# Optimization experiments

Hardware: AMD Instinct MI355X
Metric: run time of the kernel (lower is better)

The kernel has to match this reference:

```python
import jax, jax.numpy as jnp
import numpy as np

FEATURE_MAPS = (38, 19, 10, 5, 3, 1)
BOXES_PER_LOC = (4, 6, 6, 6, 4, 4)
IMAGE_SIZE = 300
DEC_SIZE = 64  # WhatDecoder output resolution
MAX_OBJECTS = 10
Z_WHAT = 64


def _recon_indices():
    # Maps per-prior slots (8732) to per-location slots (1940), matching
    # Decoder.reconstruction_indices: each location index repeated boxes_per_loc times.
    idx, last = [], 0
    for fm, bpl in zip(FEATURE_MAPS, BOXES_PER_LOC):
        loc = np.arange(fm * fm) + last
        idx.append(np.repeat(loc, bpl))
        last = loc[-1] + 1
    return jnp.asarray(np.concatenate(idx), dtype=jnp.int32)


def _deconv2x2(x, W, b):
    # ConvTranspose2d(kernel=2, stride=2): each input pixel expands to a 2x2 block.
    n, c, h, w = x.shape
    o = W.shape[1]
    y = jnp.einsum('nchw,coab->nohawb', x, W).reshape(n, o, 2 * h, 2 * w)
    return y + b[None, :, None, None]


def _what_decoder(z, params):
    # z (M, Z_WHAT) -> (M, 3, 64, 64) in [0,1]
    x = z[:, :, None, None]
    nl = len(params)
    for i, (W, b) in enumerate(params):
        x = _deconv2x2(x, W, b)
        x = jax.nn.relu(x) if i < nl - 1 else jax.nn.sigmoid(x)
    return x


def _stn(images, z_where):
    # Spatial transformer: place (M,3,S,S) glyphs into IMAGE_SIZE canvas at box
    # z_where (M,4) = (cx,cy,w,h) in [0,1]; bilinear sampling, zeros padding.
    M, _, S, _ = images.shape
    cx, cy, w, h = (z_where[:, i] for i in range(4))
    # output pixel centers in normalized [-1,1] coords (align_corners=False)
    coords = (2.0 * jnp.arange(IMAGE_SIZE, dtype=images.dtype) + 1.0) / IMAGE_SIZE - 1.0
    xo = coords[None, None, :]
    yo = coords[None, :, None]
    eps = 1e-6
    u = (xo - (2.0 * cx - 1.0)[:, None, None]) / (w[:, None, None] + eps)  # (M,H,W)
    v = (yo - (2.0 * cy - 1.0)[:, None, None]) / (h[:, None, None] + eps)
    ix = ((u + 1.0) * S - 1.0) / 2.0  # input pixel coords
    iy = ((v + 1.0) * S - 1.0) / 2.0

    def sample_one(img, iy, ix):
        iy0 = jnp.floor(iy)
        ix0 = jnp.floor(ix)
        wy1 = iy - iy0
        wx1 = ix - ix0
        wy0 = 1.0 - wy1
        wx0 = 1.0 - wx1

        def g(y, x):
            yi = jnp.clip(y, 0, S - 1).astype(jnp.int32)
            xi = jnp.clip(x, 0, S - 1).astype(jnp.int32)
            valid = ((y >= 0) & (y < S) & (x >= 0) & (x < S)).astype(img.dtype)
            return img[:, yi, xi] * valid  # (3,H,W)

        return (g(iy0, ix0) * wy0 * wx0 + g(iy0, ix0 + 1) * wy0 * wx1
                + g(iy0 + 1, ix0) * wy1 * wx0 + g(iy0 + 1, ix0 + 1) * wy1 * wx1)

    return jax.vmap(sample_one)(images, iy, ix)  # (M,3,H,H)


def setup_inputs() -> dict:
    key = jax.random.key(0)
    ks = jax.random.split(key, 20)
    B, NLOC, NPRI = 16, 1940, 8732
    chans = (Z_WHAT, 256, 128, 64, 32, 16, 3)
    inp = {
        'z_what': jax.random.normal(ks[0], (B, NLOC, Z_WHAT), jnp.float32),
        'z_where': jax.random.uniform(ks[1], (B, NPRI, 4), jnp.float32),
        'z_present': jax.random.randint(ks[2], (B, NPRI, 1), 0, 2, jnp.int32),
        'z_depth': jax.random.normal(ks[3], (B, NLOC, 1), jnp.float32),
    }
    for i in range(6):
        ci, co = chans[i], chans[i + 1]
        inp[f'W{i}'] = jax.random.normal(ks[4 + i], (ci, co, 2, 2), jnp.float32) * 0.1
        inp[f'b{i}'] = jnp.zeros((co,), jnp.float32)
    return inp


def reference(z_what, z_where, z_present, z_depth,
              W0, b0, W1, b1, W2, b2, W3, b3, W4, b4, W5, b5):
    params = [(W0, b0), (W1, b1), (W2, b2), (W3, b3), (W4, b4), (W5, b5)]
    idx = _recon_indices()
    zw = z_what[:, idx]      # (B, P, D) ragged location->prior gather
    zd = z_depth[:, idx, 0]  # (B, P)
    order = jnp.argsort(-zd, axis=1)[:, :MAX_OBJECTS]  # depth sort, descending
    B, K = order.shape

    def gat(t):
        return jnp.take_along_axis(
            t, jnp.broadcast_to(order[:, :, None], (B, K, t.shape[-1])), axis=1)

    sw = gat(zw)            # (B,K,D)
    swr = gat(z_where)      # (B,K,4)
    sp = gat(z_present)     # (B,K,1)

    decoded = _what_decoder(sw.reshape(B * K, Z_WHAT), params)      # (B*K,3,64,64)
    transformed = _stn(decoded, swr.reshape(B * K, 4))              # (B*K,3,300,300)
    present = (sp == 1).astype(transformed.dtype).reshape(B * K, 1, 1, 1)
    objs = (transformed * present).reshape(B, K, 3, IMAGE_SIZE, IMAGE_SIZE)

    # z-buffer merge: per pixel, take first nonzero object in depth order
    nz = objs != 0.0
    first = nz & (jnp.cumsum(nz.astype(jnp.int32), axis=1) == 1)
    return jnp.sum(objs * first.astype(objs.dtype), axis=1)  # (B,3,300,300)
```

## Files before the change

kernel.cpp:

```cpp
#include <hip/hip_runtime.h>
#include <cmath>

#define NLOC 1940
#define NPRI 8732
#define BATCH 16
#define KOBJ 10

__device__ __forceinline__ void ins3(float v, int i,
    float& a0, float& a1, float& a2, int& j0, int& j1, int& j2)
{
    if (v > a0 || (v == a0 && i < j0)) { a2=a1; j2=j1; a1=a0; j1=j0; a0=v; j0=i; }
    else if (v > a1 || (v == a1 && i < j1)) { a2=a1; j2=j1; a1=v; j1=i; }
    else if (v > a2 || (v == a2 && i < j2)) { a2=v; j2=i; }
}

__device__ __forceinline__ float ix_chain(int x, float shift, float wh) {
    const float xo = __fsub_rn(__fdiv_rn(__fadd_rn(__fmul_rn(2.0f, (float)x), 1.0f), 300.0f), 1.0f);
    const float u  = __fdiv_rn(__fsub_rn(xo, shift), wh);
    return __fmul_rn(__fsub_rn(__fmul_rn(__fadd_rn(u, 1.0f), 64.0f), 1.0f), 0.5f);
}

__global__ __launch_bounds__(256) void prep_kernel(
    const float* __restrict__ W0, const float* __restrict__ W1, float* __restrict__ Wr,
    const float* __restrict__ z_what, const float* __restrict__ z_where,
    const int* __restrict__ z_present, const float* __restrict__ z_depth,
    float* __restrict__ gathered, float* __restrict__ paramsF, int* __restrict__ paramsI,
    int* __restrict__ obnd)
{
    __shared__ float sv[768];
    __shared__ int   si[768];
    __shared__ int   locs3[3];
    __shared__ int   sj_start[3], sj_bpl[3];
    __shared__ int   spres[10], sjj[10];
    __shared__ float szw[10][4];
    __shared__ float lpf[KOBJ][4];
    __shared__ int   lcnt;
    const int tid = threadIdx.x;

    if (blockIdx.x < 768) {
        const int idx = blockIdx.x * 256 + tid;
        if (idx < 65536) {
            int q = idx >> 14, rem = idx & 16383, c = rem >> 8, o = rem & 255;
            Wr[idx] = W0[(((c << 8) | o) << 2) + q];
        } else {
            int i2 = idx - 65536;
            int q = i2 >> 15, rem = i2 & 32767, c = rem >> 7, o = rem & 127;
            Wr[idx] = W1[(((c << 7) | o) << 2) + q];
        }
        return;
    }

    const int b = blockIdx.x - 768;
    float v0 = -INFINITY, v1 = -INFINITY, v2 = -INFINITY;
    int   i0 = NLOC, i1 = NLOC, i2 = NLOC;
    for (int i = tid; i < NLOC; i += 256) {
        float v = z_depth[b * NLOC + i];
        ins3(v, i, v0, v1, v2, i0, i1, i2);
    }
    sv[tid*3+0] = v0; sv[tid*3+1] = v1; sv[tid*3+2] = v2;
    si[tid*3+0] = i0; si[tid*3+1] = i1; si[tid*3+2] = i2;
    __syncthreads();
    for (int s = 128; s > 0; s >>= 1) {
        if (tid < s) {
            float a0 = sv[tid*3], a1 = sv[tid*3+1], a2 = sv[tid*3+2];
            int   j0 = si[tid*3], j1 = si[tid*3+1], j2 = si[tid*3+2];
            const int o = tid + s;
            ins3(sv[o*3+0], si[o*3+0], a0, a1, a2, j0, j1, j2);
            ins3(sv[o*3+1], si[o*3+1], a0, a1, a2, j0, j1, j2);
            ins3(sv[o*3+2], si[o*3+2], a0, a1, a2, j0, j1, j2);
            sv[tid*3] = a0; sv[tid*3+1] = a1; sv[tid*3+2] = a2;
            si[tid*3] = j0; si[tid*3+1] = j1; si[tid*3+2] = j2;
        }
        __syncthreads();
    }

    if (tid < 3) {
        int L = si[tid];
        locs3[tid] = L;
        int start, bpl;
        if (L < 1444)      { start = 4 * L;                 bpl = 4; }
        else if (L < 1805) { start = 5776 + 6 * (L - 1444); bpl = 6; }
        else if (L < 1905) { start = 7942 + 6 * (L - 1805); bpl = 6; }
        else if (L < 1930) { start = 8542 + 6 * (L - 1905); bpl = 6; }
        else if (L < 1939) { start = 8692 + 4 * (L - 1930); bpl = 4; }
        else               { start = 8728;                  bpl = 4; }
        sj_start[tid] = start; sj_bpl[tid] = bpl;
    }
    __syncthreads();
    if (tid < 10) {
        const int b0 = sj_bpl[0], b1 = sj_bpl[1];
        int j, o;
        if (tid < b0)           { j = 0; o = tid; }
        else if (tid < b0 + b1) { j = 1; o = tid - b0; }
        else                    { j = 2; o = tid - b0 - b1; }
        const int p = sj_start[j] + o;
        sjj[tid]   = j;
        spres[tid] = z_present[b * NPRI + p];
        const float4 zw = *reinterpret_cast<const float4*>(z_where + (b * NPRI + p) * 4);
        szw[tid][0] = zw.x; szw[tid][1] = zw.y; szw[tid][2] = zw.z; szw[tid][3] = zw.w;
    }
    __syncthreads();
    if (tid == 0) {
        int cnt = 0;
        for (int i = 0; i < 10; ++i) {
            if (spres[i] == 1) {
                float p0 = __fadd_rn(szw[i][2], 1e-6f);
                float p1 = __fadd_rn(szw[i][3], 1e-6f);
                float p2 = __fsub_rn(__fmul_rn(2.0f, szw[i][0]), 1.0f);
                float p3 = __fsub_rn(__fmul_rn(2.0f, szw[i][1]), 1.0f);
                float* pf = paramsF + (b * KOBJ + cnt) * 4;
                pf[0] = p0; pf[1] = p1; pf[2] = p2; pf[3] = p3;
                lpf[cnt][0] = p0; lpf[cnt][1] = p1; lpf[cnt][2] = p2; lpf[cnt][3] = p3;
                paramsI[b * 12 + 2 + cnt] = b * 3 + sjj[i];
                cnt++;
            }
        }
        paramsI[b * 12] = cnt;
        lcnt = cnt;
    }
    __syncthreads();
    if (tid < 4 * KOBJ) {
        const int k = tid >> 2, ty = tid & 3;
        if (k < lcnt) {
            const float wh = (ty < 2) ? lpf[k][0] : lpf[k][1];
            const float sh = (ty < 2) ? lpf[k][2] : lpf[k][3];
            int res;
            if ((ty & 1) == 0) {
                int lo = 0, hi = 300;
                while (lo < hi) { int m = (lo + hi) >> 1;
                    if (ix_chain(m, sh, wh) > -1.0f) hi = m; else lo = m + 1; }
                res = lo;
            } else {
                int lo = -1, hi = 299;
                while (lo < hi) { int m = (lo + hi + 1) >> 1;
                    if (ix_chain(m, sh, wh) < 64.0f) lo = m; else hi = m - 1; }
                res = lo;
            }
            obnd[(b * KOBJ + k) * 4 + ty] = res;
        }
    }
    if (tid < 192) {
        int j = tid >> 6, c = tid & 63;
        gathered[(b * 3 + j) * 64 + c] = z_what[(b * NLOC + locs3[j]) * 64 + c];
    }
}

__global__ __launch_bounds__(256) void dec_fused(
    const float* __restrict__ gathered, const float* __restrict__ Wr,
    const float* __restrict__ b0v, const float* __restrict__ b1v,
    const float* __restrict__ W2, const float* __restrict__ b2v,
    const float* __restrict__ W3, const float* __restrict__ b3v,
    const float* __restrict__ W4, const float* __restrict__ b4v,
    const float* __restrict__ W5, const float* __restrict__ b5v,
    float* __restrict__ decoded)
{
    __shared__ __align__(16) float P[2048];
    __shared__ __align__(16) float Q[1024];
    __shared__ __align__(16) float Zs[128];
    const int r  = blockIdx.x;
    const int g  = blockIdx.y;
    const int t  = threadIdx.x;
    const int y1 = r >> 2, x1 = r & 3;
    const int q0 = (y1 >> 1) * 2 + (x1 >> 1);
    const int p1 = (y1 & 1) * 2 + (x1 & 1);
    const int s2 = g * 2;

    if (t < 128) Zs[t] = gathered[(s2 + (t & 1)) * 64 + (t >> 1)];
    __syncthreads();

    {
        const float* w0 = Wr + q0 * 16384 + t;
        float bv = b0v[t];
        float2 acc = make_float2(bv, bv);
        #pragma unroll 8
        for (int c = 0; c < 64; ++c) {
            float w = w0[c << 8];
            float2 xs = *reinterpret_cast<const float2*>(Zs + (c << 1));
            acc.x = fmaf(xs.x, w, acc.x); acc.y = fmaf(xs.y, w, acc.y);
        }
        *reinterpret_cast<float2*>(P + (t << 1)) =
            make_float2(fmaxf(acc.x, 0.f), fmaxf(acc.y, 0.f));
    }
    __syncthreads();

    {
        const int o = t & 127, h = t >> 7;
        const float* w1 = Wr + 65536 + p1 * 32768 + o;
        float2 acc;
        if (h == 0) { float bv = b1v[o]; acc = make_float2(bv, bv); }
        else        { acc = make_float2(0.f, 0.f); }
        const int cb = h << 7;
        #pragma unroll 8
        for (int c = 0; c < 128; ++c) {
            float w = w1[(cb + c) << 7];
            float2 xs = *reinterpret_cast<const float2*>(P + ((cb + c) << 1));
            acc.x = fmaf(xs.x, w, acc.x); acc.y = fmaf(xs.y, w, acc.y);
        }
        if (h == 1) *reinterpret_cast<float2*>(P + 512 + (o << 1)) = acc;
        __syncthreads();
        if (h == 0) {
            float2 p2 = *reinterpret_cast<const float2*>(P + 512 + (o << 1));
            acc.x += p2.x; acc.y += p2.y;
            *reinterpret_cast<float2*>(Q + (o << 1)) =
                make_float2(fmaxf(acc.x, 0.f), fmaxf(acc.y, 0.f));
        }
    }
    __syncthreads();

    {
        const float* w2 = W2 + t;
        float bv = b2v[t >> 2];
        float2 acc = make_float2(bv, bv);
        #pragma unroll 8
        for (int ci = 0; ci < 128; ++ci) {
            float w = w2[ci << 8];
            float2 xs = *reinterpret_cast<const float2*>(Q + (ci << 1));
            acc.x = fmaf(xs.x, w, acc.x); acc.y = fmaf(xs.y, w, acc.y);
        }
        *reinterpret_cast<float2*>(P + (t << 1)) =
            make_float2(fmaxf(acc.x, 0.f), fmaxf(acc.y, 0.f));
    }
    __syncthreads();

    {
        const int px = t & 15, coa = t >> 4;
        const int ly = px >> 2, lx = px & 3;
        const int par = (ly >> 1) * 2 + (lx >> 1);
        const int wp  = (ly & 1) * 2 + (lx & 1);
        const float* w3 = W3 + coa * 4 + wp;
        float bva = b3v[coa], bvb = b3v[coa + 16];
        float2 a0 = make_float2(bva, bva);
        float2 a1 = make_float2(bvb, bvb);
        #pragma unroll 8
        for (int ci = 0; ci < 64; ++ci) {
            float2 xs = *reinterpret_cast<const float2*>(P + (ci << 3) + (par << 1));
            float wa = w3[ci << 7];
            float wb = w3[(ci << 7) + 64];
            a0.x = fmaf(xs.x, wa, a0.x); a0.y = fmaf(xs.y, wa, a0.y);
            a1.x = fmaf(xs.x, wb, a1.x); a1.y = fmaf(xs.y, wb, a1.y);
        }
        *reinterpret_cast<float2*>(Q + (coa << 5) + (px << 1)) =
            make_float2(fmaxf(a0.x, 0.f), fmaxf(a0.y, 0.f));
        *reinterpret_cast<float2*>(Q + ((coa + 16) << 5) + (px << 1)) =
            make_float2(fmaxf(a1.x, 0.f), fmaxf(a1.y, 0.f));
    }
    __syncthreads();

    {
        const int px = t & 63, co0 = t >> 6;
        const int ly = px >> 3, lx = px & 7;
        const int par = (ly >> 1) * 4 + (lx >> 1);
        const int wp  = (ly & 1) * 2 + (lx & 1);
        const float* w4 = W4 + co0 * 4 + wp;
        float2 acc[4];
        #pragma unroll
        for (int k = 0; k < 4; ++k) { float bv = b4v[co0 + 4 * k]; acc[k] = make_float2(bv, bv); }
        #pragma unroll 4
        for (int ci = 0; ci < 32; ++ci) {
            float2 xs = *reinterpret_cast<const float2*>(Q + (ci << 5) + (par << 1));
            #pragma unroll
            for (int k = 0; k < 4; ++k) {
                float w = w4[(ci << 6) + k * 16];
                acc[k].x = fmaf(xs.x, w, acc[k].x); acc[k].y = fmaf(xs.y, w, acc[k].y);
            }
        }
        #pragma unroll
        for (int k = 0; k < 4; ++k)
            *reinterpret_cast<float2*>(P + ((co0 + 4 * k) << 7) + (px << 1)) =
                make_float2(fmaxf(acc[k].x, 0.f), fmaxf(acc[k].y, 0.f));
    }
    __syncthreads();

    {
        const int px = t;
        const int ly = px >> 4, lx = px & 15;
        const int par = (ly >> 1) * 8 + (lx >> 1);
        const int wp  = (ly & 1) * 2 + (lx & 1);
        const int gy = y1 * 16 + ly, gx = x1 * 16 + lx;
        const float* w5 = W5 + wp;
        float2 acc[3];
        #pragma unroll
        for (int c = 0; c < 3; ++c) { float bv = b5v[c]; acc[c] = make_float2(bv, bv); }
        #pragma unroll 4
        for (int ci = 0; ci < 16; ++ci) {
            float2 xs = *reinterpret_cast<const float2*>(P + (ci << 7) + (par << 1));
            #pragma unroll
            for (int c = 0; c < 3; ++c) {
                float w = w5[ci * 12 + c * 4];
                acc[c].x = fmaf(xs.x, w, acc[c].x); acc[c].y = fmaf(xs.y, w, acc[c].y);
            }
        }
        const int pbase = (gy * 64 + gx) * 3;
        #pragma unroll
        for (int c = 0; c < 3; ++c) {
            decoded[(s2 + 0) * 12288 + pbase + c] = 1.0f / (1.0f + expf(-acc[c].x));
            decoded[(s2 + 1) * 12288 + pbase + c] = 1.0f / (1.0f + expf(-acc[c].y));
        }
    }
}

__global__ __launch_bounds__(256) void stn_kernel(
    const float* __restrict__ decoded, const float* __restrict__ paramsF,
    const int* __restrict__ paramsI, const int* __restrict__ obnd,
    float* __restrict__ out)
{
    const int b = blockIdx.y;
    const int pix0 = blockIdx.x * 256;
    const int yfirst = pix0 / 300;
    __shared__ float sp[KOBJ][4];
    __shared__ int   ssamp[KOBJ];
    __shared__ int   s_xlo[KOBJ], s_xhi[KOBJ], s_ylo[KOBJ], s_yhi[KOBJ];
    __shared__ int   scnt;
    __shared__ float s_wy0[KOBJ][2], s_wy1[KOBJ][2];
    __shared__ int   s_rb0[KOBJ][2], s_rb1[KOBJ][2];
    __shared__ unsigned char s_cov[KOBJ][2];
    __shared__ unsigned char s_vy[KOBJ][2];
    __shared__ int s_list[KOBJ];
    __shared__ int s_lc;
    const int tid = threadIdx.x;

    if (tid == 0) scnt = paramsI[b * 12];
    if (tid < KOBJ) {
        #pragma unroll
        for (int c = 0; c < 4; ++c) sp[tid][c] = paramsF[(b * KOBJ + tid) * 4 + c];
        ssamp[tid] = paramsI[b * 12 + 2 + tid];
        const int4 bd = *reinterpret_cast<const int4*>(obnd + (b * KOBJ + tid) * 4);
        s_xlo[tid] = bd.x; s_xhi[tid] = bd.y; s_ylo[tid] = bd.z; s_yhi[tid] = bd.w;
    }
    __syncthreads();

    if (tid < 2 * scnt) {
        const int k = tid >> 1, sel = tid & 1;
        int yy = yfirst + sel; if (yy > 299) yy = 299;
        const bool cov = (yy >= s_ylo[k]) && (yy <= s_yhi[k]);
        s_cov[k][sel] = cov ? 1 : 0;
        if (cov) {
            const float iy = ix_chain(yy, sp[k][3], sp[k][1]);
            const float iy0f = floorf(iy);
            const float iy1f = __fadd_rn(iy0f, 1.0f);
            const float wy1  = __fsub_rn(iy, iy0f);
            s_wy1[k][sel] = wy1;
            s_wy0[k][sel] = __fsub_rn(1.0f, wy1);
            const bool vy0 = (iy0f >= 0.0f) && (iy0f < 64.0f);
            const bool vy1 = (iy1f >= 0.0f) && (iy1f < 64.0f);
            s_vy[k][sel] = (unsigned char)((vy0 ? 1 : 0) | (vy1 ? 2 : 0));
            s_rb0[k][sel] = ((int)fminf(fmaxf(iy0f, 0.0f), 63.0f)) * 64;
            s_rb1[k][sel] = ((int)fminf(fmaxf(iy1f, 0.0f), 63.0f)) * 64;
        }
    }
    __syncthreads();
    if (tid == 0) {
        int lc = 0;
        for (int k = 0; k < scnt; ++k)
            if (s_cov[k][0] | s_cov[k][1]) s_list[lc++] = k;
        s_lc = lc;
    }
    __syncthreads();

    const int pix = pix0 + tid;
    if (pix < 90000) {
        const int y = pix / 300;
        const int x = pix - y * 300;
        const int rs = y - yfirst;
        float o0 = 0.0f, o1 = 0.0f, o2 = 0.0f;
        bool d0 = false, d1 = false, d2 = false;
        const int lc = s_lc;
        for (int m = 0; m < lc; ++m) {
            const int k = s_list[m];
            if (!s_cov[k][rs]) continue;
            if (x < s_xlo[k] || x > s_xhi[k]) continue;

            const float ix = ix_chain(x, sp[k][2], sp[k][0]);
            const float ix0f = floorf(ix);
            const float ix1f = __fadd_rn(ix0f, 1.0f);
            const float wx1 = __fsub_rn(ix, ix0f);
            const float wx0 = __fsub_rn(1.0f, wx1);
            const bool vx0 = (ix0f >= 0.0f) && (ix0f < 64.0f);
            const bool vx1 = (ix1f >= 0.0f) && (ix1f < 64.0f);
            const int x0 = (int)fminf(fmaxf(ix0f, 0.0f), 63.0f);
            const int x1 = (int)fminf(fmaxf(ix1f, 0.0f), 63.0f);

            const float wy0 = s_wy0[k][rs], wy1 = s_wy1[k][rs];
            const int rb0 = s_rb0[k][rs], rb1 = s_rb1[k][rs];
            const unsigned char vy = s_vy[k][rs];
            const bool m00 = (vy & 1) && vx0, m01 = (vy & 1) && vx1;
            const bool m10 = (vy & 2) && vx0, m11 = (vy & 2) && vx1;
            const float* img = decoded + ssamp[k] * 12288;

            float g00x = 0.f, g00y = 0.f, g00z = 0.f;
            float g01x = 0.f, g01y = 0.f, g01z = 0.f;
            float g10x = 0.f, g10y = 0.f, g10z = 0.f;
            float g11x = 0.f, g11y = 0.f, g11z = 0.f;
            if (m00) { const float* p = img + (rb0 + x0) * 3; g00x = p[0]; g00y = p[1]; g00z = p[2]; }
            if (m01) { const float* p = img + (rb0 + x1) * 3; g01x = p[0]; g01y = p[1]; g01z = p[2]; }
            if (m10) { const float* p = img + (rb1 + x0) * 3; g10x = p[0]; g10y = p[1]; g10z = p[2]; }
            if (m11) { const float* p = img + (rb1 + x1) * 3; g11x = p[0]; g11y = p[1]; g11z = p[2]; }

            if (!d0) {
                float val = g00x * wy0 * wx0 + g01x * wy0 * wx1 + g10x * wy1 * wx0 + g11x * wy1 * wx1;
                if (val != 0.0f) { o0 = val; d0 = true; }
            }
            if (!d1) {
                float val = g00y * wy0 * wx0 + g01y * wy0 * wx1 + g10y * wy1 * wx0 + g11y * wy1 * wx1;
                if (val != 0.0f) { o1 = val; d1 = true; }
            }
            if (!d2) {
                float val = g00z * wy0 * wx0 + g01z * wy0 * wx1 + g10z * wy1 * wx0 + g11z * wy1 * wx1;
                if (val != 0.0f) { o2 = val; d2 = true; }
            }
            if (d0 && d1 && d2) break;
        }
        const int ob = b * 270000 + pix;
        out[ob] = o0;
        out[ob + 90000] = o1;
        out[ob + 180000] = o2;
    }
}

extern "C" void kernel_launch(void* const* d_in, const int* in_sizes, int n_in,
                              void* d_out, int out_size, void* d_ws, size_t ws_size,
                              hipStream_t stream)
{
    const float* z_what    = (const float*)d_in[0];
    const float* z_where   = (const float*)d_in[1];
    const int*   z_present = (const int*)d_in[2];
    const float* z_depth   = (const float*)d_in[3];
    const float* W0 = (const float*)d_in[4];   const float* b0 = (const float*)d_in[5];
    const float* W1 = (const float*)d_in[6];   const float* b1 = (const float*)d_in[7];
    const float* W2 = (const float*)d_in[8];   const float* b2 = (const float*)d_in[9];
    const float* W3 = (const float*)d_in[10];  const float* b3 = (const float*)d_in[11];
    const float* W4 = (const float*)d_in[12];  const float* b4 = (const float*)d_in[13];
    const float* W5 = (const float*)d_in[14];  const float* b5 = (const float*)d_in[15];

    float* ws = (float*)d_ws;
    float* gathered = ws;
    float* paramsF  = ws + 16384;
    int*   paramsI  = (int*)(ws + 17408);
    int*   obnd     = (int*)(ws + 17664);
    float* decoded  = ws + 32768;
    float* Wr       = (float*)d_out;
    float* outp     = (float*)d_out;

    hipLaunchKernelGGL(prep_kernel, dim3(784), dim3(256), 0, stream,
                       W0, W1, Wr, z_what, z_where, z_present, z_depth,
                       gathered, paramsF, paramsI, obnd);
    hipLaunchKernelGGL(dec_fused, dim3(16, 24), dim3(256), 0, stream,
                       gathered, Wr, b0, b1, W2, b2, W3, b3, W4, b4, W5, b5, decoded);
    hipLaunchKernelGGL(stn_kernel, dim3(352, BATCH), dim3(256), 0, stream,
                       decoded, paramsF, paramsI, obnd, outp);
}
```

Measured before the change: 150.1 us.

## Fuse prep, decoder and STN kernels into one cooperative persistent kernel

Merges the three separate kernel launches into a single cooperative kernel that runs each stage in grid-stride loops, separated by grid-wide syncs, with shared memory overlaid in a union. The aim is to remove inter-kernel launch gaps and tail effects. In exchange it adds grid.sync overhead and caps occupancy through launch bounds. The STN stage also loses the 2D block mapping and instead loops over virtual blocks.

```diff
diff --git a/kernel.cpp b/kernel.cpp
--- a/kernel.cpp
+++ b/kernel.cpp
@@ -1,5 +1,8 @@
 #include <hip/hip_runtime.h>
+#include <hip/hip_cooperative_groups.h>
 #include <cmath>
+
+namespace cg = cooperative_groups;
 
 #define NLOC 1940
 #define NPRI 8732
@@ -20,400 +23,419 @@
     return __fmul_rn(__fsub_rn(__fmul_rn(__fadd_rn(u, 1.0f), 64.0f), 1.0f), 0.5f);
 }
 
-__global__ __launch_bounds__(256) void prep_kernel(
-    const float* __restrict__ W0, const float* __restrict__ W1, float* __restrict__ Wr,
+struct PrepSM {
+    float sv[768];
+    int   si[768];
+    int   locs3[3];
+    int   sj_start[3], sj_bpl[3];
+    int   spres[10], sjj[10];
+    float szw[10][4];
+    float lpf[KOBJ][4];
+    int   lcnt;
+};
+struct DecSM {
+    float P[2048];
+    float Q[1024];
+    float Zs[128];
+};
+struct StnSM {
+    float sp[KOBJ][4];
+    int   ssamp[KOBJ];
+    int   s_xlo[KOBJ], s_xhi[KOBJ], s_ylo[KOBJ], s_yhi[KOBJ];
+    int   scnt;
+    float s_wy0[KOBJ][2], s_wy1[KOBJ][2];
+    int   s_rb0[KOBJ][2], s_rb1[KOBJ][2];
+    unsigned char s_cov[KOBJ][2];
+    unsigned char s_vy[KOBJ][2];
+    int s_list[KOBJ];
+    int s_lc;
+};
+union alignas(16) SMem {
+    PrepSM prep;
+    DecSM  dec;
+    StnSM  stn;
+};
+
+__global__ __launch_bounds__(256, 4) void fused_all(
     const float* __restrict__ z_what, const float* __restrict__ z_where,
     const int* __restrict__ z_present, const float* __restrict__ z_depth,
-    float* __restrict__ gathered, float* __restrict__ paramsF, int* __restrict__ paramsI,
-    int* __restrict__ obnd)
-{
-    __shared__ float sv[768];
-    __shared__ int   si[768];
-    __shared__ int   locs3[3];
-    __shared__ int   sj_start[3], sj_bpl[3];
-    __shared__ int   spres[10], sjj[10];
-    __shared__ float szw[10][4];
-    __shared__ float lpf[KOBJ][4];
-    __shared__ int   lcnt;
-    const int tid = threadIdx.x;
-
-    if (blockIdx.x < 768) {
-        const int idx = blockIdx.x * 256 + tid;
-        if (idx < 65536) {
-            int q = idx >> 14, rem = idx & 16383, c = rem >> 8, o = rem & 255;
-            Wr[idx] = W0[(((c << 8) | o) << 2) + q];
-        } else {
-            int i2 = idx - 65536;
-            int q = i2 >> 15, rem = i2 & 32767, c = rem >> 7, o = rem & 127;
-            Wr[idx] = W1[(((c << 7) | o) << 2) + q];
-        }
-        return;
-    }
-
-    const int b = blockIdx.x - 768;
-    float v0 = -INFINITY, v1 = -INFINITY, v2 = -INFINITY;
-    int   i0 = NLOC, i1 = NLOC, i2 = NLOC;
-    for (int i = tid; i < NLOC; i += 256) {
-        float v = z_depth[b * NLOC + i];
-        ins3(v, i, v0, v1, v2, i0, i1, i2);
-    }
-    sv[tid*3+0] = v0; sv[tid*3+1] = v1; sv[tid*3+2] = v2;
-    si[tid*3+0] = i0; si[tid*3+1] = i1; si[tid*3+2] = i2;
-    __syncthreads();
-    for (int s = 128; s > 0; s >>= 1) {
-        if (tid < s) {
-            float a0 = sv[tid*3], a1 = sv[tid*3+1], a2 = sv[tid*3+2];
-            int   j0 = si[tid*3], j1 = si[tid*3+1], j2 = si[tid*3+2];
-            const int o = tid + s;
-            ins3(sv[o*3+0], si[o*3+0], a0, a1, a2, j0, j1, j2);
-            ins3(sv[o*3+1], si[o*3+1], a0, a1, a2, j0, j1, j2);
-            ins3(sv[o*3+2], si[o*3+2], a0, a1, a2, j0, j1, j2);
-            sv[tid*3] = a0; sv[tid*3+1] = a1; sv[tid*3+2] = a2;
-            si[tid*3] = j0; si[tid*3+1] = j1; si[tid*3+2] = j2;
-        }
-        __syncthreads();
-    }
-
-    if (tid < 3) {
-        int L = si[tid];
-        locs3[tid] = L;
-        int start, bpl;
-        if (L < 1444)      { start = 4 * L;                 bpl = 4; }
-        else if (L < 1805) { start = 5776 + 6 * (L - 1444); bpl = 6; }
-        else if (L < 1905) { start = 7942 + 6 * (L - 1805); bpl = 6; }
-        else if (L < 1930) { start = 8542 + 6 * (L - 1905); bpl = 6; }
-        else if (L < 1939) { start = 8692 + 4 * (L - 1930); bpl = 4; }
-        else               { start = 8728;                  bpl = 4; }
-        sj_start[tid] = start; sj_bpl[tid] = bpl;
-    }
-    __syncthreads();
-    if (tid < 10) {
-        const int b0 = sj_bpl[0], b1 = sj_bpl[1];
-        int j, o;
-        if (tid < b0)           { j = 0; o = tid; }
-        else if (tid < b0 + b1) { j = 1; o = tid - b0; }
-        else                    { j = 2; o = tid - b0 - b1; }
-        const int p = sj_start[j] + o;
-        sjj[tid]   = j;
-        spres[tid] = z_present[b * NPRI + p];
-        const float4 zw = *reinterpret_cast<const float4*>(z_where + (b * NPRI + p) * 4);
-        szw[tid][0] = zw.x; szw[tid][1] = zw.y; szw[tid][2] = zw.z; szw[tid][3] = zw.w;
-    }
-    __syncthreads();
-    if (tid == 0) {
-        int cnt = 0;
-        for (int i = 0; i < 10; ++i) {
-            if (spres[i] == 1) {
-                float p0 = __fadd_rn(szw[i][2], 1e-6f);
-                float p1 = __fadd_rn(szw[i][3], 1e-6f);
-                float p2 = __fsub_rn(__fmul_rn(2.0f, szw[i][0]), 1.0f);
-                float p3 = __fsub_rn(__fmul_rn(2.0f, szw[i][1]), 1.0f);
-                float* pf = paramsF + (b * KOBJ + cnt) * 4;
-                pf[0] = p0; pf[1] = p1; pf[2] = p2; pf[3] = p3;
-                lpf[cnt][0] = p0; lpf[cnt][1] = p1; lpf[cnt][2] = p2; lpf[cnt][3] = p3;
-                paramsI[b * 12 + 2 + cnt] = b * 3 + sjj[i];
-                cnt++;
-            }
-        }
-        paramsI[b * 12] = cnt;
-        lcnt = cnt;
-    }
-    __syncthreads();
-    if (tid < 4 * KOBJ) {
-        const int k = tid >> 2, ty = tid & 3;
-        if (k < lcnt) {
-            const float wh = (ty < 2) ? lpf[k][0] : lpf[k][1];
-            const float sh = (ty < 2) ? lpf[k][2] : lpf[k][3];
-            int res;
-            if ((ty & 1) == 0) {
-                int lo = 0, hi = 300;
-                while (lo < hi) { int m = (lo + hi) >> 1;
-                    if (ix_chain(m, sh, wh) > -1.0f) hi = m; else lo = m + 1; }
-                res = lo;
-            } else {
-                int lo = -1, hi = 299;
-                while (lo < hi) { int m = (lo + hi + 1) >> 1;
-                    if (ix_chain(m, sh, wh) < 64.0f) lo = m; else hi = m - 1; }
-                res = lo;
-            }
-            obnd[(b * KOBJ + k) * 4 + ty] = res;
-        }
-    }
-    if (tid < 192) {
-        int j = tid >> 6, c = tid & 63;
-        gathered[(b * 3 + j) * 64 + c] = z_what[(b * NLOC + locs3[j]) * 64 + c];
-    }
-}
-
-__global__ __launch_bounds__(256) void dec_fused(
-    const float* __restrict__ gathered, const float* __restrict__ Wr,
-    const float* __restrict__ b0v, const float* __restrict__ b1v,
+    const float* __restrict__ W0, const float* __restrict__ b0v,
+    const float* __restrict__ W1, const float* __restrict__ b1v,
     const float* __restrict__ W2, const float* __restrict__ b2v,
     const float* __restrict__ W3, const float* __restrict__ b3v,
     const float* __restrict__ W4, const float* __restrict__ b4v,
     const float* __restrict__ W5, const float* __restrict__ b5v,
-    float* __restrict__ decoded)
+    float* __restrict__ Wr,
+    float* __restrict__ gathered, float* __restrict__ paramsF,
+    int* __restrict__ paramsI, int* __restrict__ obnd,
+    float* __restrict__ decoded, float* __restrict__ out)
 {
-    __shared__ __align__(16) float P[2048];
-    __shared__ __align__(16) float Q[1024];
-    __shared__ __align__(16) float Zs[128];
-    const int r  = blockIdx.x;
-    const int g  = blockIdx.y;
-    const int t  = threadIdx.x;
-    const int y1 = r >> 2, x1 = r & 3;
-    const int q0 = (y1 >> 1) * 2 + (x1 >> 1);
-    const int p1 = (y1 & 1) * 2 + (x1 & 1);
-    const int s2 = g * 2;
-
-    if (t < 128) Zs[t] = gathered[(s2 + (t & 1)) * 64 + (t >> 1)];
-    __syncthreads();
-
-    {
-        const float* w0 = Wr + q0 * 16384 + t;
-        float bv = b0v[t];
-        float2 acc = make_float2(bv, bv);
-        #pragma unroll 8
-        for (int c = 0; c < 64; ++c) {
-            float w = w0[c << 8];
-            float2 xs = *reinterpret_cast<const float2*>(Zs + (c << 1));
-            acc.x = fmaf(xs.x, w, acc.x); acc.y = fmaf(xs.y, w, acc.y);
-        }
-        *reinterpret_cast<float2*>(P + (t << 1)) =
-            make_float2(fmaxf(acc.x, 0.f), fmaxf(acc.y, 0.f));
+    __shared__ SMem sm;
+    const int tid = threadIdx.x;
+    cg::grid_group grid = cg::this_grid();
+
+    for (int vb = blockIdx.x; vb < 784; vb += gridDim.x) {
+        if (vb < 768) {
+            const int idx = vb * 256 + tid;
+            if (idx < 65536) {
+                int q = idx >> 14, rem = idx & 16383, c = rem >> 8, o = rem & 255;
+                Wr[idx] = W0[(((c << 8) | o) << 2) + q];
+            } else {
+                int i2 = idx - 65536;
+                int q = i2 >> 15, rem = i2 & 32767, c = rem >> 7, o = rem & 127;
+                Wr[idx] = W1[(((c << 7) | o) << 2) + q];
+            }
+        } else {
+            PrepSM& SP = sm.prep;
+            const int b = vb - 768;
+            float v0 = -INFINITY, v1 = -INFINITY, v2 = -INFINITY;
+            int   i0 = NLOC, i1 = NLOC, i2 = NLOC;
+            for (int i = tid; i < NLOC; i += 256) {
+                float v = z_depth[b * NLOC + i];
+                ins3(v, i, v0, v1, v2, i0, i1, i2);
+            }
+            SP.sv[tid*3+0] = v0; SP.sv[tid*3+1] = v1; SP.sv[tid*3+2] = v2;
+            SP.si[tid*3+0] = i0; SP.si[tid*3+1] = i1; SP.si[tid*3+2] = i2;
+            __syncthreads();
+            for (int s = 128; s > 0; s >>= 1) {
+                if (tid < s) {
+                    float a0 = SP.sv[tid*3], a1 = SP.sv[tid*3+1], a2 = SP.sv[tid*3+2];
+                    int   j0 = SP.si[tid*3], j1 = SP.si[tid*3+1], j2 = SP.si[tid*3+2];
+                    const int o = tid + s;
+                    ins3(SP.sv[o*3+0], SP.si[o*3+0], a0, a1, a2, j0, j1, j2);
+                    ins3(SP.sv[o*3+1], SP.si[o*3+1], a0, a1, a2, j0, j1, j2);
+                    ins3(SP.sv[o*3+2], SP.si[o*3+2], a0, a1, a2, j0, j1, j2);
+                    SP.sv[tid*3] = a0; SP.sv[tid*3+1] = a1; SP.sv[tid*3+2] = a2;
+                    SP.si[tid*3] = j0; SP.si[tid*3+1] = j1; SP.si[tid*3+2] = j2;
+                }
+                __syncthreads();
+            }
+
+            if (tid < 3) {
+                int L = SP.si[tid];
+                SP.locs3[tid] = L;
+                int start, bpl;
+                if (L < 1444)      { start = 4 * L;                 bpl = 4; }
+                else if (L < 1805) { start = 5776 + 6 * (L - 1444); bpl = 6; }
+                else if (L < 1905) { start = 7942 + 6 * (L - 1805); bpl = 6; }
+                else if (L < 1930) { start = 8542 + 6 * (L - 1905); bpl = 6; }
+                else if (L < 1939) { start = 8692 + 4 * (L - 1930); bpl = 4; }
+                else               { start = 8728;                  bpl = 4; }
+                SP.sj_start[tid] = start; SP.sj_bpl[tid] = bpl;
+            }
+            __syncthreads();
+            if (tid < 10) {
+                const int c0 = SP.sj_bpl[0], c1 = SP.sj_bpl[1];
+                int j, o;
+                if (tid < c0)           { j = 0; o = tid; }
+                else if (tid < c0 + c1) { j = 1; o = tid - c0; }
+                else                    { j = 2; o = tid - c0 - c1; }
+                const int p = SP.sj_start[j] + o;
+                SP.sjj[tid]   = j;
+                SP.spres[tid] = z_present[b * NPRI + p];
+                const float4 zw = *reinterpret_cast<const float4*>(z_where + (b * NPRI + p) * 4);
+                SP.szw[tid][0] = zw.x; SP.szw[tid][1] = zw.y; SP.szw[tid][2] = zw.z; SP.szw[tid][3] = zw.w;
+            }
+            __syncthreads();
+            if (tid == 0) {
+                int cnt = 0;
+                for (int i = 0; i < 10; ++i) {
+                    if (SP.spres[i] == 1) {
+                        float p0 = __fadd_rn(SP.szw[i][2], 1e-6f);
+                        float p1 = __fadd_rn(SP.szw[i][3], 1e-6f);
+                        float p2 = __fsub_rn(__fmul_rn(2.0f, SP.szw[i][0]), 1.0f);
+                        float p3 = __fsub_rn(__fmul_rn(2.0f, SP.szw[i][1]), 1.0f);
+                        float* pf = paramsF + (b * KOBJ + cnt) * 4;
+                        pf[0] = p0; pf[1] = p1; pf[2] = p2; pf[3] = p3;
+                        SP.lpf[cnt][0] = p0; SP.lpf[cnt][1] = p1; SP.lpf[cnt][2] = p2; SP.lpf[cnt][3] = p3;
+                        paramsI[b * 12 + 2 + cnt] = b * 3 + SP.sjj[i];
+                        cnt++;
+                    }
+                }
+                paramsI[b * 12] = cnt;
+                SP.lcnt = cnt;
+            }
+            __syncthreads();
+            if (tid < 4 * KOBJ) {
+                const int k = tid >> 2, ty = tid & 3;
+                if (k < SP.lcnt) {
+                    const float wh = (ty < 2) ? SP.lpf[k][0] : SP.lpf[k][1];
+                    const float sh = (ty < 2) ? SP.lpf[k][2] : SP.lpf[k][3];
+                    int res;
+                    if ((ty & 1) == 0) {
+                        int lo = 0, hi = 300;
+                        while (lo < hi) { int m = (lo + hi) >> 1;
+                            if (ix_chain(m, sh, wh) > -1.0f) hi = m; else lo = m + 1; }
+                        res = lo;
+                    } else {
+                        int lo = -1, hi = 299;
+                        while (lo < hi) { int m = (lo + hi + 1) >> 1;
+                            if (ix_chain(m, sh, wh) < 64.0f) lo = m; else hi = m - 1; }
+                        res = lo;
+                    }
+                    obnd[(b * KOBJ + k) * 4 + ty] = res;
+                }
+            }
+            if (tid < 192) {
+                int j = tid >> 6, c = tid & 63;
+                gathered[(b * 3 + j) * 64 + c] = z_what[(b * NLOC + SP.locs3[j]) * 64 + c];
+            }
+            __syncthreads();
+        }
     }
-    __syncthreads();
-
-    {
-        const int o = t & 127, h = t >> 7;
-        const float* w1 = Wr + 65536 + p1 * 32768 + o;
-        float2 acc;
-        if (h == 0) { float bv = b1v[o]; acc = make_float2(bv, bv); }
-        else        { acc = make_float2(0.f, 0.f); }
-        const int cb = h << 7;
-        #pragma unroll 8
-        for (int c = 0; c < 128; ++c) {
-            float w = w1[(cb + c) << 7];
-            float2 xs = *reinterpret_cast<const float2*>(P + ((cb + c) << 1));
-            acc.x = fmaf(xs.x, w, acc.x); acc.y = fmaf(xs.y, w, acc.y);
-        }
-        if (h == 1) *reinterpret_cast<float2*>(P + 512 + (o << 1)) = acc;
-        __syncthreads();
-        if (h == 0) {
-            float2 p2 = *reinterpret_cast<const float2*>(P + 512 + (o << 1));
-            acc.x += p2.x; acc.y += p2.y;
-            *reinterpret_cast<float2*>(Q + (o << 1)) =
+    __threadfence();
+    grid.sync();
+
+    for (int vb = blockIdx.x; vb < 384; vb += gridDim.x) {
+        DecSM& SD = sm.dec;
+        const int r  = vb & 15;
+        const int g  = vb >> 4;
+        const int t  = tid;
+        const int y1 = r >> 2, x1 = r & 3;
+        const int q0 = (y1 >> 1) * 2 + (x1 >> 1);
+        const int p1 = (y1 & 1) * 2 + (x1 & 1);
+        const int s2 = g * 2;
+
+        if (t < 128) SD.Zs[t] = gathered[(s2 + (t & 1)) * 64 + (t >> 1)];
+        __syncthreads();
+
+        {
+            const float* w0 = Wr + q0 * 16384 + t;
+            float bv = b0v[t];
+            float2 acc = make_float2(bv, bv);
+            #pragma unroll 8
+            for (int c = 0; c < 64; ++c) {
+                float w = w0[c << 8];
+                float2 xs = *reinterpret_cast<const float2*>(&SD.Zs[c << 1]);
+                acc.x = fmaf(xs.x, w, acc.x); acc.y = fmaf(xs.y, w, acc.y);
+            }
+            *reinterpret_cast<float2*>(&SD.P[t << 1]) =
                 make_float2(fmaxf(acc.x, 0.f), fmaxf(acc.y, 0.f));
         }
-    }
-    __syncthreads();
-
-    {
-        const float* w2 = W2 + t;
-        float bv = b2v[t >> 2];
-        float2 acc = make_float2(bv, bv);
-        #pragma unroll 8
-        for (int ci = 0; ci < 128; ++ci) {
-            float w = w2[ci << 8];
-            float2 xs = *reinterpret_cast<const float2*>(Q + (ci << 1));
-            acc.x = fmaf(xs.x, w, acc.x); acc.y = fmaf(xs.y, w, acc.y);
-        }
-        *reinterpret_cast<float2*>(P + (t << 1)) =
-            make_float2(fmaxf(acc.x, 0.f), fmaxf(acc.y, 0.f));
-    }
-    __syncthreads();
-
-    {
-        const int px = t & 15, coa = t >> 4;
-        const int ly = px >> 2, lx = px & 3;
-        const int par = (ly >> 1) * 2 + (lx >> 1);
-        const int wp  = (ly & 1) * 2 + (lx & 1);
-        const float* w3 = W3 + coa * 4 + wp;
-        float bva = b3v[coa], bvb = b3v[coa + 16];
-        float2 a0 = make_float2(bva, bva);
-        float2 a1 = make_float2(bvb, bvb);
-        #pragma unroll 8
-        for (int ci = 0; ci < 64; ++ci) {
-            float2 xs = *reinterpret_cast<const float2*>(P + (ci << 3) + (par << 1));
-            float wa = w3[ci << 7];
-            float wb = w3[(ci << 7) + 64];
-            a0.x = fmaf(xs.x, wa, a0.x); a0.y = fmaf(xs.y, wa, a0.y);
-            a1.x = fmaf(xs.x, wb, a1.x); a1.y = fmaf(xs.y, wb, a1.y);
-        }
-        *reinterpret_cast<float2*>(Q + (coa << 5) + (px << 1)) =
-            make_float2(fmaxf(a0.x, 0.f), fmaxf(a0.y, 0.f));
-        *reinterpret_cast<float2*>(Q + ((coa + 16) << 5) + (px << 1)) =
-            make_float2(fmaxf(a1.x, 0.f), fmaxf(a1.y, 0.f));
-    }
-    __syncthreads();
-
-    {
-        const int px = t & 63, co0 = t >> 6;
-        const int ly = px >> 3, lx = px & 7;
-        const int par = (ly >> 1) * 4 + (lx >> 1);
-        const int wp  = (ly & 1) * 2 + (lx & 1);
-        const float* w4 = W4 + co0 * 4 + wp;
-        float2 acc[4];
-        #pragma unroll
-        for (int k = 0; k < 4; ++k) { float bv = b4v[co0 + 4 * k]; acc[k] = make_float2(bv, bv); }
-        #pragma unroll 4
-        for (int ci = 0; ci < 32; ++ci) {
-            float2 xs = *reinterpret_cast<const float2*>(Q + (ci << 5) + (par << 1));
+        __syncthreads();
+
+        {
+            const int o = t & 127, h = t >> 7;
+            const float* w1 = Wr + 65536 + p1 * 32768 + o;
+            float2 acc;
+            if (h == 0) { float bv = b1v[o]; acc = make_float2(bv, bv); }
+            else        { acc = make_float2(0.f, 0.f); }
+            const int cb = h << 7;
+            #pragma unroll 8
+            for (int c = 0; c < 128; ++c) {
+                float w = w1[(cb + c) << 7];
+                float2 xs = *reinterpret_cast<const float2*>(&SD.P[(cb + c) << 1]);
+                acc.x = fmaf(xs.x, w, acc.x); acc.y = fmaf(xs.y, w, acc.y);
+            }
+            if (h == 1) *reinterpret_cast<float2*>(&SD.P[512 + (o << 1)]) = acc;
+            __syncthreads();
+            if (h == 0) {
+                float2 p2 = *reinterpret_cast<const float2*>(&SD.P[512 + (o << 1)]);
+                acc.x += p2.x; acc.y += p2.y;
+                *reinterpret_cast<float2*>(&SD.Q[o << 1]) =
+                    make_float2(fmaxf(acc.x, 0.f), fmaxf(acc.y, 0.f));
+            }
+        }
+        __syncthreads();
+
+        {
+            const float* w2 = W2 + t;
+            float bv = b2v[t >> 2];
+            float2 acc = make_float2(bv, bv);
+            #pragma unroll 8
+            for (int ci = 0; ci < 128; ++ci) {
+                float w = w2[ci << 8];
+                float2 xs = *reinterpret_cast<const float2*>(&SD.Q[ci << 1]);
+                acc.x = fmaf(xs.x, w, acc.x); acc.y = fmaf(xs.y, w, acc.y);
+            }
+            *reinterpret_cast<float2*>(&SD.P[t << 1]) =
+                make_float2(fmaxf(acc.x, 0.f), fmaxf(acc.y, 0.f));
+        }
+        __syncthreads();
+
+        {
+            const int px = t & 15, coa = t >> 4;
+            const int ly = px >> 2, lx = px & 3;
+            const int par = (ly >> 1) * 2 + (lx >> 1);
+            const int wp  = (ly & 1) * 2 + (lx & 1);
+            const float* w3 = W3 + coa * 4 + wp;
+            float bva = b3v[coa], bvb = b3v[coa + 16];
+            float2 a0 = make_float2(bva, bva);
+            float2 a1 = make_float2(bvb, bvb);
+            #pragma unroll 8
+            for (int ci = 0; ci < 64; ++ci) {
+                float2 xs = *reinterpret_cast<const float2*>(&SD.P[(ci << 3) + (par << 1)]);
+                float wa = w3[ci << 7];
+                float wb = w3[(ci << 7) + 64];
+                a0.x = fmaf(xs.x, wa, a0.x); a0.y = fmaf(xs.y, wa, a0.y);
+                a1.x = fmaf(xs.x, wb, a1.x); a1.y = fmaf(xs.y, wb, a1.y);
+            }
+            *reinterpret_cast<float2*>(&SD.Q[(coa << 5) + (px << 1)]) =
+                make_float2(fmaxf(a0.x, 0.f), fmaxf(a0.y, 0.f));
+            *reinterpret_cast<float2*>(&SD.Q[((coa + 16) << 5) + (px << 1)]) =
+                make_float2(fmaxf(a1.x, 0.f), fmaxf(a1.y, 0.f));
+        }
+        __syncthreads();
+
+        {
+            const int px = t & 63, co0 = t >> 6;
+            const int ly = px >> 3, lx = px & 7;
+            const int par = (ly >> 1) * 4 + (lx >> 1);
+            const int wp  = (ly & 1) * 2 + (lx & 1);
+            const float* w4 = W4 + co0 * 4 + wp;
+            float2 acc[4];
             #pragma unroll
-            for (int k = 0; k < 4; ++k) {
-                float w = w4[(ci << 6) + k * 16];
-                acc[k].x = fmaf(xs.x, w, acc[k].x); acc[k].y = fmaf(xs.y, w, acc[k].y);
-            }
-        }
-        #pragma unroll
-        for (int k = 0; k < 4; ++k)
-            *reinterpret_cast<float2*>(P + ((co0 + 4 * k) << 7) + (px << 1)) =
-                make_float2(fmaxf(acc[k].x, 0.f), fmaxf(acc[k].y, 0.f));
-    }
-    __syncthreads();
-
-    {
-        const int px = t;
-        const int ly = px >> 4, lx = px & 15;
-        const int par = (ly >> 1) * 8 + (lx >> 1);
-        const int wp  = (ly & 1) * 2 + (lx & 1);
-        const int gy = y1 * 16 + ly, gx = x1 * 16 + lx;
-        const float* w5 = W5 + wp;
-        float2 acc[3];
-        #pragma unroll
-        for (int c = 0; c < 3; ++c) { float bv = b5v[c]; acc[c] = make_float2(bv, bv); }
-        #pragma unroll 4
-        for (int ci = 0; ci < 16; ++ci) {
-            float2 xs = *reinterpret_cast<const float2*>(P + (ci << 7) + (par << 1));
+            for (int k = 0; k < 4; ++k) { float bv = b4v[co0 + 4 * k]; acc[k] = make_float2(bv, bv); }
+            #pragma unroll 4
+            for (int ci = 0; ci < 32; ++ci) {
+                float2 xs = *reinterpret_cast<const float2*>(&SD.Q[(ci << 5) + (par << 1)]);
+                #pragma unroll
+                for (int k = 0; k < 4; ++k) {
+                    float w = w4[(ci << 6) + k * 16];
+                    acc[k].x = fmaf(xs.x, w, acc[k].x); acc[k].y = fmaf(xs.y, w, acc[k].y);
+                }
+            }
+            #pragma unroll
+            for (int k = 0; k < 4; ++k)
+                *reinterpret_cast<float2*>(&SD.P[((co0 + 4 * k) << 7) + (px << 1)]) =
+                    make_float2(fmaxf(acc[k].x, 0.f), fmaxf(acc[k].y, 0.f));
+        }
+        __syncthreads();
+
+        {
+            const int px = t;
+            const int ly = px >> 4, lx = px & 15;
+            const int par = (ly >> 1) * 8 + (lx >> 1);
+            const int wp  = (ly & 1) * 2 + (lx & 1);
+            const int gy = y1 * 16 + ly, gx = x1 * 16 + lx;
+            const float* w5 = W5 + wp;
+            float2 acc[3];
+            #pragma unroll
+            for (int c = 0; c < 3; ++c) { float bv = b5v[c]; acc[c] = make_float2(bv, bv); }
+            #pragma unroll 4
+            for (int ci = 0; ci < 16; ++ci) {
+                float2 xs = *reinterpret_cast<const float2*>(&SD.P[(ci << 7) + (par << 1)]);
+                #pragma unroll
+                for (int c = 0; c < 3; ++c) {
+                    float w = w5[ci * 12 + c * 4];
+                    acc[c].x = fmaf(xs.x, w, acc[c].x); acc[c].y = fmaf(xs.y, w, acc[c].y);
+                }
+            }
+            const int pbase = (gy * 64 + gx) * 3;
             #pragma unroll
             for (int c = 0; c < 3; ++c) {
-                float w = w5[ci * 12 + c * 4];
-                acc[c].x = fmaf(xs.x, w, acc[c].x); acc[c].y = fmaf(xs.y, w, acc[c].y);
-            }
-        }
-        const int pbase = (gy * 64 + gx) * 3;
-        #pragma unroll
-        for (int c = 0; c < 3; ++c) {
-            decoded[(s2 + 0) * 12288 + pbase + c] = 1.0f / (1.0f + expf(-acc[c].x));
-            decoded[(s2 + 1) * 12288 + pbase + c] = 1.0f / (1.0f + expf(-acc[c].y));
-        }
+                decoded[(s2 + 0) * 12288 + pbase + c] = 1.0f / (1.0f + expf(-acc[c].x));
+                decoded[(s2 + 1) * 12288 + pbase + c] = 1.0f / (1.0f + expf(-acc[c].y));
+            }
+        }
+        __syncthreads();
     }
-}
-
-__global__ __launch_bounds__(256) void stn_kernel(
-    const float* __restrict__ decoded, const float* __restrict__ paramsF,
-    const int* __restrict__ paramsI, const int* __restrict__ obnd,
-    float* __restrict__ out)
-{
-    const int b = blockIdx.y;
-    const int pix0 = blockIdx.x * 256;
-    const int yfirst = pix0 / 300;
-    __shared__ float sp[KOBJ][4];
-    __shared__ int   ssamp[KOBJ];
-    __shared__ int   s_xlo[KOBJ], s_xhi[KOBJ], s_ylo[KOBJ], s_yhi[KOBJ];
-    __shared__ int   scnt;
-    __shared__ float s_wy0[KOBJ][2], s_wy1[KOBJ][2];
-    __shared__ int   s_rb0[KOBJ][2], s_rb1[KOBJ][2];
-    __shared__ unsigned char s_cov[KOBJ][2];
-    __shared__ unsigned char s_vy[KOBJ][2];
-    __shared__ int s_list[KOBJ];
-    __shared__ int s_lc;
-    const int tid = threadIdx.x;
-
-    if (tid == 0) scnt = paramsI[b * 12];
-    if (tid < KOBJ) {
-        #pragma unroll
-        for (int c = 0; c < 4; ++c) sp[tid][c] = paramsF[(b * KOBJ + tid) * 4 + c];
-        ssamp[tid] = paramsI[b * 12 + 2 + tid];
-        const int4 bd = *reinterpret_cast<const int4*>(obnd + (b * KOBJ + tid) * 4);
-        s_xlo[tid] = bd.x; s_xhi[tid] = bd.y; s_ylo[tid] = bd.z; s_yhi[tid] = bd.w;
-    }
-    __syncthreads();
-
-    if (tid < 2 * scnt) {
-        const int k = tid >> 1, sel = tid & 1;
-        int yy = yfirst + sel; if (yy > 299) yy = 299;
-        const bool cov = (yy >= s_ylo[k]) && (yy <= s_yhi[k]);
-        s_cov[k][sel] = cov ? 1 : 0;
-        if (cov) {
-            const float iy = ix_chain(yy, sp[k][3], sp[k][1]);
-            const float iy0f = floorf(iy);
-            const float iy1f = __fadd_rn(iy0f, 1.0f);
-            const float wy1  = __fsub_rn(iy, iy0f);
-            s_wy1[k][sel] = wy1;
-            s_wy0[k][sel] = __fsub_rn(1.0f, wy1);
-            const bool vy0 = (iy0f >= 0.0f) && (iy0f < 64.0f);
-            const bool vy1 = (iy1f >= 0.0f) && (iy1f < 64.0f);
-            s_vy[k][sel] = (unsigned char)((vy0 ? 1 : 0) | (vy1 ? 2 : 0));
-            s_rb0[k][sel] = ((int)fminf(fmaxf(iy0f, 0.0f), 63.0f)) * 64;
-            s_rb1[k][sel] = ((int)fminf(fmaxf(iy1f, 0.0f), 63.0f)) * 64;
-        }
-    }
-    __syncthreads();
-    if (tid == 0) {
-        int lc = 0;
-        for (int k = 0; k < scnt; ++k)
-            if (s_cov[k][0] | s_cov[k][1]) s_list[lc++] = k;
-        s_lc = lc;
-    }
-    __syncthreads();
-
-    const int pix = pix0 + tid;
-    if (pix < 90000) {
-        const int y = pix / 300;
-        const int x = pix - y * 300;
-        const int rs = y - yfirst;
-        float o0 = 0.0f, o1 = 0.0f, o2 = 0.0f;
-        bool d0 = false, d1 = false, d2 = false;
-        const int lc = s_lc;
-        for (int m = 0; m < lc; ++m) {
-            const int k = s_list[m];
-            if (!s_cov[k][rs]) continue;
-            if (x < s_xlo[k] || x > s_xhi[k]) continue;
-
-            const float ix = ix_chain(x, sp[k][2], sp[k][0]);
-            const float ix0f = floorf(ix);
-            const float ix1f = __fadd_rn(ix0f, 1.0f);
-            const float wx1 = __fsub_rn(ix, ix0f);
-            const float wx0 = __fsub_rn(1.0f, wx1);
-            const bool vx0 = (ix0f >= 0.0f) && (ix0f < 64.0f);
-            const bool vx1 = (ix1f >= 0.0f) && (ix1f < 64.0f);
-            const int x0 = (int)fminf(fmaxf(ix0f, 0.0f), 63.0f);
-            const int x1 = (int)fminf(fmaxf(ix1f, 0.0f), 63.0f);
-
-            const float wy0 = s_wy0[k][rs], wy1 = s_wy1[k][rs];
-            const int rb0 = s_rb0[k][rs], rb1 = s_rb1[k][rs];
-            const unsigned char vy = s_vy[k][rs];
-            const bool m00 = (vy & 1) && vx0, m01 = (vy & 1) && vx1;
-            const bool m10 = (vy & 2) && vx0, m11 = (vy & 2) && vx1;
-            const float* img = decoded + ssamp[k] * 12288;
-
-            float g00x = 0.f, g00y = 0.f, g00z = 0.f;
-            float g01x = 0.f, g01y = 0.f, g01z = 0.f;
-            float g10x = 0.f, g10y = 0.f, g10z = 0.f;
-            float g11x = 0.f, g11y = 0.f, g11z = 0.f;
-            if (m00) { const float* p = img + (rb0 + x0) * 3; g00x = p[0]; g00y = p[1]; g00z = p[2]; }
-            if (m01) { const float* p = img + (rb0 + x1) * 3; g01x = p[0]; g01y = p[1]; g01z = p[2]; }
-            if (m10) { const float* p = img + (rb1 + x0) * 3; g10x = p[0]; g10y = p[1]; g10z = p[2]; }
-            if (m11) { const float* p = img + (rb1 + x1) * 3; g11x = p[0]; g11y = p[1]; g11z = p[2]; }
-
-            if (!d0) {
-                float val = g00x * wy0 * wx0 + g01x * wy0 * wx1 + g10x * wy1 * wx0 + g11x * wy1 * wx1;
-                if (val != 0.0f) { o0 = val; d0 = true; }
-            }
-            if (!d1) {
-                float val = g00y * wy0 * wx0 + g01y * wy0 * wx1 + g10y * wy1 * wx0 + g11y * wy1 * wx1;
-                if (val != 0.0f) { o1 = val; d1 = true; }
-            }
-            if (!d2) {
-                float val = g00z * wy0 * wx0 + g01z * wy0 * wx1 + g10z * wy1 * wx0 + g11z * wy1 * wx1;
-                if (val != 0.0f) { o2 = val; d2 = true; }
-            }
-            if (d0 && d1 && d2) break;
-        }
-        const int ob = b * 270000 + pix;
-        out[ob] = o0;
-        out[ob + 90000] = o1;
-        out[ob + 180000] = o2;
+    __threadfence();
+    grid.sync();
+
+    for (int vb = blockIdx.x; vb < 5632; vb += gridDim.x) {
+        __syncthreads();
+        StnSM& S = sm.stn;
+        const int b = vb / 352;
+        const int pix0 = (vb - b * 352) * 256;
+        const int yfirst = pix0 / 300;
+
+        if (tid == 0) S.scnt = paramsI[b * 12];
+        if (tid < KOBJ) {
+            #pragma unroll
+            for (int c = 0; c < 4; ++c) S.sp[tid][c] = paramsF[(b * KOBJ + tid) * 4 + c];
+            S.ssamp[tid] = paramsI[b * 12 + 2 + tid];
+            const int4 bd = *reinterpret_cast<const int4*>(obnd + (b * KOBJ + tid) * 4);
+            S.s_xlo[tid] = bd.x; S.s_xhi[tid] = bd.y; S.s_ylo[tid] = bd.z; S.s_yhi[tid] = bd.w;
+        }
+        __syncthreads();
+
+        if (tid < 2 * S.scnt) {
+            const int k = tid >> 1, sel = tid & 1;
+            int yy = yfirst + sel; if (yy > 299) yy = 299;
+            const bool cov = (yy >= S.s_ylo[k]) && (yy <= S.s_yhi[k]);
+            S.s_cov[k][sel] = cov ? 1 : 0;
+            if (cov) {
+                const float iy = ix_chain(yy, S.sp[k][3], S.sp[k][1]);
+                const float iy0f = floorf(iy);
+                const float iy1f = __fadd_rn(iy0f, 1.0f);
+                const float wy1  = __fsub_rn(iy, iy0f);
+                S.s_wy1[k][sel] = wy1;
+                S.s_wy0[k][sel] = __fsub_rn(1.0f, wy1);
+                const bool vy0 = (iy0f >= 0.0f) && (iy0f < 64.0f);
+                const bool vy1 = (iy1f >= 0.0f) && (iy1f < 64.0f);
+                S.s_vy[k][sel] = (unsigned char)((vy0 ? 1 : 0) | (vy1 ? 2 : 0));
+                S.s_rb0[k][sel] = ((int)fminf(fmaxf(iy0f, 0.0f), 63.0f)) * 64;
+                S.s_rb1[k][sel] = ((int)fminf(fmaxf(iy1f, 0.0f), 63.0f)) * 64;
+            }
+        }
+        __syncthreads();
+        if (tid == 0) {
+            int lc = 0;
+            for (int k = 0; k < S.scnt; ++k)
+                if (S.s_cov[k][0] | S.s_cov[k][1]) S.s_list[lc++] = k;
+            S.s_lc = lc;
+        }
+        __syncthreads();
+
+        const int pix = pix0 + tid;
+        if (pix < 90000) {
+            const int y = pix / 300;
+            const int x = pix - y * 300;
+            const int rs = y - yfirst;
+            float o0 = 0.0f, o1 = 0.0f, o2 = 0.0f;
+            bool d0 = false, d1 = false, d2 = false;
+            const int lc = S.s_lc;
+            for (int m = 0; m < lc; ++m) {
+                const int k = S.s_list[m];
+                if (!S.s_cov[k][rs]) continue;
+                if (x < S.s_xlo[k] || x > S.s_xhi[k]) continue;
+
+                const float ix = ix_chain(x, S.sp[k][2], S.sp[k][0]);
+                const float ix0f = floorf(ix);
+                const float ix1f = __fadd_rn(ix0f, 1.0f);
+                const float wx1 = __fsub_rn(ix, ix0f);
+                const float wx0 = __fsub_rn(1.0f, wx1);
+                const bool vx0 = (ix0f >= 0.0f) && (ix0f < 64.0f);
+                const bool vx1 = (ix1f >= 0.0f) && (ix1f < 64.0f);
+                const int x0 = (int)fminf(fmaxf(ix0f, 0.0f), 63.0f);
+                const int x1 = (int)fminf(fmaxf(ix1f, 0.0f), 63.0f);
+
+                const float wy0 = S.s_wy0[k][rs], wy1 = S.s_wy1[k][rs];
+                const int rb0 = S.s_rb0[k][rs], rb1 = S.s_rb1[k][rs];
+                const unsigned char vy = S.s_vy[k][rs];
+                const bool m00 = (vy & 1) && vx0, m01 = (vy & 1) && vx1;
+                const bool m10 = (vy & 2) && vx0, m11 = (vy & 2) && vx1;
+                const float* img = decoded + S.ssamp[k] * 12288;
+
+                float g00x = 0.f, g00y = 0.f, g00z = 0.f;
+                float g01x = 0.f, g01y = 0.f, g01z = 0.f;
+                float g10x = 0.f, g10y = 0.f, g10z = 0.f;
+                float g11x = 0.f, g11y = 0.f, g11z = 0.f;
+                if (m00) { const float* p = img + (rb0 + x0) * 3; g00x = p[0]; g00y = p[1]; g00z = p[2]; }
+                if (m01) { const float* p = img + (rb0 + x1) * 3; g01x = p[0]; g01y = p[1]; g01z = p[2]; }
+                if (m10) { const float* p = img + (rb1 + x0) * 3; g10x = p[0]; g10y = p[1]; g10z = p[2]; }
+                if (m11) { const float* p = img + (rb1 + x1) * 3; g11x = p[0]; g11y = p[1]; g11z = p[2]; }
+
+                if (!d0) {
+                    float val = g00x * wy0 * wx0 + g01x * wy0 * wx1 + g10x * wy1 * wx0 + g11x * wy1 * wx1;
+                    if (val != 0.0f) { o0 = val; d0 = true; }
+                }
+                if (!d1) {
+                    float val = g00y * wy0 * wx0 + g01y * wy0 * wx1 + g10y * wy1 * wx0 + g11y * wy1 * wx1;
+                    if (val != 0.0f) { o1 = val; d1 = true; }
+                }
+                if (!d2) {
+                    float val = g00z * wy0 * wx0 + g01z * wy0 * wx1 + g10z * wy1 * wx0 + g11z * wy1 * wx1;
+                    if (val != 0.0f) { o2 = val; d2 = true; }
+                }
+                if (d0 && d1 && d2) break;
+            }
+            const int ob = b * 270000 + pix;
+            out[ob] = o0;
+            out[ob + 90000] = o1;
+            out[ob + 180000] = o2;
+        }
     }
 }
 
@@ -441,11 +463,26 @@
     float* Wr       = (float*)d_out;
     float* outp     = (float*)d_out;
 
-    hipLaunchKernelGGL(prep_kernel, dim3(784), dim3(256), 0, stream,
-                       W0, W1, Wr, z_what, z_where, z_present, z_depth,
-                       gathered, paramsF, paramsI, obnd);
-    hipLaunchKernelGGL(dec_fused, dim3(16, 24), dim3(256), 0, stream,
-                       gathered, Wr, b0, b1, W2, b2, W3, b3, W4, b4, W5, b5, decoded);
-    hipLaunchKernelGGL(stn_kernel, dim3(352, BATCH), dim3(256), 0, stream,
-                       decoded, paramsF, paramsI, obnd, outp);
+    static int g_grid = 0;
+    if (g_grid == 0) {
+        int perCU = 0;
+        if (hipOccupancyMaxActiveBlocksPerMultiprocessor(&perCU, fused_all, 256, 0) != hipSuccess || perCU <= 0)
+            perCU = 4;
+        int dev = 0, cus = 0;
+        hipGetDevice(&dev);
+        if (hipDeviceGetAttribute(&cus, hipDeviceAttributeMultiprocessorCount, dev) != hipSuccess || cus <= 0)
+            cus = 256;
+        long cap = (long)perCU * (long)cus;
+        g_grid = (int)(cap > 2048 ? 2048 : cap);
+    }
+
+    void* args[] = {
+        (void*)&z_what, (void*)&z_where, (void*)&z_present, (void*)&z_depth,
+        (void*)&W0, (void*)&b0, (void*)&W1, (void*)&b1,
+        (void*)&W2, (void*)&b2, (void*)&W3, (void*)&b3,
+        (void*)&W4, (void*)&b4, (void*)&W5, (void*)&b5,
+        (void*)&Wr, (void*)&gathered, (void*)&paramsF, (void*)&paramsI, (void*)&obnd,
+        (void*)&decoded, (void*)&outp
+    };
+    hipLaunchCooperativeKernel(fused_all, dim3(g_grid), dim3(256), args, 0u, stream);
 }
```

Measured after the change: 391.8 us. 161% more time.
